# Optimization experiments

Hardware: AMD Instinct MI355X
Metric: run time of the kernel (lower is better)

Reference implementation:

```python
import jax, jax.numpy as jnp
import numpy as np

B, S, D, H, DFF = 4, 1024, 1024, 16, 4096
MAX_LEN = 1024
DK = D // H
EPS = 1e-5


def _ln(x, g, b):
    m = jnp.mean(x, axis=-1, keepdims=True)
    v = jnp.mean(jnp.square(x - m), axis=-1, keepdims=True)
    return (x - m) / jnp.sqrt(v + EPS) * g + b


def setup_inputs() -> dict:
    key = jax.random.key(0)
    ks = jax.random.split(key, 16)
    s = 0.02
    inp = {
        "x": jax.random.normal(ks[0], (B, S, D), jnp.float32),
        "wq": jax.random.normal(ks[1], (D, D), jnp.float32) * s,
        "bq": jnp.zeros((D,), jnp.float32),
        "wk": jax.random.normal(ks[2], (D, D), jnp.float32) * s,
        "bk": jnp.zeros((D,), jnp.float32),
        "wv": jax.random.normal(ks[3], (D, D), jnp.float32) * s,
        "bv": jnp.zeros((D,), jnp.float32),
        "wo": jax.random.normal(ks[4], (D, D), jnp.float32) * s,
        "bo": jnp.zeros((D,), jnp.float32),
        "rel_table": jax.random.normal(ks[5], (2 * MAX_LEN - 1, H), jnp.float32) * s,
        "ln1_g": jnp.ones((D,), jnp.float32),
        "ln1_b": jnp.zeros((D,), jnp.float32),
        "w1": jax.random.normal(ks[6], (D, DFF), jnp.float32) * s,
        "b1": jnp.zeros((DFF,), jnp.float32),
        "w2": jax.random.normal(ks[7], (DFF, D), jnp.float32) * s,
        "b2": jnp.zeros((D,), jnp.float32),
        "ln2_g": jnp.ones((D,), jnp.float32),
        "ln2_b": jnp.zeros((D,), jnp.float32),
        "mask": jnp.ones((B, 1, 1, S), jnp.int32),
    }
    return inp


def reference(x, wq, bq, wk, bk, wv, bv, wo, bo, rel_table,
              ln1_g, ln1_b, w1, b1, w2, b2, ln2_g, ln2_b, mask):
    # --- multi-head attention with relative position bias (post-LN encoder layer, eval mode) ---
    q = (x @ wq + bq).reshape(B, S, H, DK).transpose(0, 2, 1, 3)  # [B,H,S,dk]
    k = (x @ wk + bk).reshape(B, S, H, DK).transpose(0, 2, 1, 3)
    v = (x @ wv + bv).reshape(B, S, H, DK).transpose(0, 2, 1, 3)

    scores = jnp.einsum('bhqd,bhkd->bhqk', q, k) / jnp.sqrt(jnp.float32(DK))

    # relative position bias: table[(q - k + max_len - 1).clip] -> [1,H,S,S]
    coords = jnp.arange(S)[:, None] - jnp.arange(S)[None, :] + (MAX_LEN - 1)
    coords = jnp.clip(coords, 0, 2 * MAX_LEN - 2)
    bias = rel_table[coords]              # [S,S,H]
    scores = scores + bias.transpose(2, 0, 1)[None]

    scores = jnp.where(mask == 0, jnp.float32(-1e9), scores)
    attn = jax.nn.softmax(scores, axis=-1)
    ctx = jnp.einsum('bhqk,bhkd->bhqd', attn, v)
    ctx = ctx.transpose(0, 2, 1, 3).reshape(B, S, D)
    attn_out = ctx @ wo + bo

    x1 = _ln(x + attn_out, ln1_g, ln1_b)

    ff = jax.nn.relu(x1 @ w1 + b1) @ w2 + b2
    return _ln(x1 + ff, ln2_g, ln2_b)
```

## Files before the change

kernel.cpp:

```cpp
#include <hip/hip_runtime.h>
#include <hip/hip_bf16.h>

typedef __hip_bfloat16 bf16;
typedef __attribute__((ext_vector_type(8))) short short8;
typedef __attribute__((ext_vector_type(4))) float f32x4;

#define LOG2E 1.4426950408889634f

typedef const __attribute__((address_space(1))) void* gptr_t;
typedef __attribute__((address_space(3))) void* sptr_t;

__device__ __forceinline__ void async16(void* lds, const void* g) {
  __builtin_amdgcn_global_load_lds((gptr_t)g, (sptr_t)lds, 16, 0, 0);
}

__device__ __forceinline__ float bf2f(unsigned short u) {
  union { unsigned int i; float f; } c; c.i = ((unsigned int)u) << 16; return c.f;
}


__global__ __launch_bounds__(256) void prep_all(
    const float* __restrict__ x, const float* __restrict__ bq,
    const float* __restrict__ bk, const float* __restrict__ bv,
    const float* __restrict__ wq, const float* __restrict__ wk,
    const float* __restrict__ wv, const float* __restrict__ wo,
    const float* __restrict__ w1, const float* __restrict__ w2,
    bf16* __restrict__ xb, float* __restrict__ bqkv,
    bf16* __restrict__ dqkv, bf16* __restrict__ dwo,
    bf16* __restrict__ dw1, bf16* __restrict__ dw2) {
  const int bid = blockIdx.x;
  if (bid < 4096) {
    int i = (bid * 256 + threadIdx.x) * 4;
    float4 v = *(const float4*)(x + i);
    bf16 h4[4] = {__float2bfloat16(v.x), __float2bfloat16(v.y),
                  __float2bfloat16(v.z), __float2bfloat16(v.w)};
    *(uint2*)((unsigned short*)xb + i) = *(uint2*)h4;
    return;
  }
  if (bid == 16384) {
#pragma unroll
    for (int j = 0; j < 12; ++j) {
      int i = j * 256 + threadIdx.x;
      bqkv[i] = (i < 1024) ? bq[i] : (i < 2048 ? bk[i - 1024] : bv[i - 2048]);
    }
    return;
  }
  __shared__ float tl[32][33];
  const int tid = bid - 4096;
  const float* s;
  bf16* d;
  int NN, KK, n0, k0;
  if (tid < 4096) {
    int m = tid >> 10, tile = tid & 1023;
    s = m == 0 ? wq : m == 1 ? wk : m == 2 ? wv : wo;
    d = m < 3 ? dqkv + (size_t)m * 1024 * 1024 : dwo;
    NN = 1024; KK = 1024;
    n0 = (tile & 31) * 32; k0 = (tile >> 5) * 32;
  } else if (tid < 8192) {
    int tile = tid - 4096;
    s = w1; d = dw1; NN = 4096; KK = 1024;
    n0 = (tile & 127) * 32; k0 = (tile >> 7) * 32;
  } else {
    int tile = tid - 8192;
    s = w2; d = dw2; NN = 1024; KK = 4096;
    n0 = (tile & 31) * 32; k0 = (tile >> 5) * 32;
  }
  const int tx = threadIdx.x & 31, ty = threadIdx.x >> 5;
#pragma unroll
  for (int j = 0; j < 4; ++j)
    tl[ty + j * 8][tx] = s[(size_t)(k0 + ty + j * 8) * NN + n0 + tx];
  __syncthreads();
#pragma unroll
  for (int j = 0; j < 4; ++j)
    d[(size_t)(n0 + ty + j * 8) * KK + k0 + tx] =
        __float2bfloat16(tl[tx][ty + j * 8]);
}

__global__ __launch_bounds__(256) void build_vt(
    const bf16* __restrict__ qkv, bf16* __restrict__ vt) {
  __shared__ bf16 tl[32][33];
  const int bhz = blockIdx.z, s0 = blockIdx.x * 32, dk0 = blockIdx.y * 32;
  const int b = bhz >> 4, h = bhz & 15;
  const int tx = threadIdx.x, ty = threadIdx.y;
#pragma unroll
  for (int j = 0; j < 4; ++j) {
    int s = s0 + ty + j * 8;
    tl[ty + j * 8][tx] =
        qkv[(size_t)(b * 1024 + s) * 3072 + 2048 + h * 64 + dk0 + tx];
  }
  __syncthreads();
#pragma unroll
  for (int j = 0; j < 4; ++j) {
    int dk = dk0 + ty + j * 8;
    vt[(size_t)(bhz * 64 + dk) * 1024 + s0 + tx] = tl[tx][ty + j * 8];
  }
}


template <int RELU>
__global__ __launch_bounds__(256) void gemm_bt(
    const bf16* __restrict__ A, const bf16* __restrict__ Bt,
    const float* __restrict__ bias, bf16* __restrict__ C, int M, int N, int K) {
  __shared__ bf16 As[2][128 * 64];
  __shared__ bf16 Bs[2][128 * 64];
  const int t = threadIdx.x;
  const int w = t >> 6, l = t & 63;
  const int m0 = blockIdx.y * 128, n0 = blockIdx.x * 128;
  const int wr = (w >> 1) * 64, wc = (w & 1) * 64;
  const int srow = l >> 3, scol = l & 7;
  const int lm = l & 15, lq = l >> 4;

  f32x4 acc[4][4];
#pragma unroll
  for (int i = 0; i < 4; ++i)
#pragma unroll
    for (int j = 0; j < 4; ++j) acc[i][j] = (f32x4){0.f, 0.f, 0.f, 0.f};

  auto stage = [&](int k0, int d) {
#pragma unroll
    for (int p = 0; p < 4; ++p) {
      int row = p * 32 + w * 8 + srow;
      int gc = scol ^ (row & 7);
      async16(&As[d][(p * 32 + w * 8) * 64], A + (size_t)(m0 + row) * K + k0 + gc * 8);
      async16(&Bs[d][(p * 32 + w * 8) * 64], Bt + (size_t)(n0 + row) * K + k0 + gc * 8);
    }
  };

  stage(0, 0);
  const int niter = K >> 6;
  for (int it = 0; it < niter; ++it) {
    const int d = it & 1;
    __syncthreads();
    short8 af[2][4], bfr[2][4];
#pragma unroll
    for (int kk = 0; kk < 2; ++kk)
#pragma unroll
      for (int mi = 0; mi < 4; ++mi) {
        int rowa = wr + mi * 16 + lm;
        af[kk][mi] = *(const short8*)&As[d][rowa * 64 + (((kk * 4 + lq) ^ (rowa & 7)) << 3)];
        int rowb = wc + mi * 16 + lm;
        bfr[kk][mi] = *(const short8*)&Bs[d][rowb * 64 + (((kk * 4 + lq) ^ (rowb & 7)) << 3)];
      }
    if (it + 1 < niter) stage((it + 1) << 6, d ^ 1);
#pragma unroll
    for (int kk = 0; kk < 2; ++kk)
#pragma unroll
      for (int mi = 0; mi < 4; ++mi)
#pragma unroll
        for (int ni = 0; ni < 4; ++ni)
          acc[mi][ni] = __builtin_amdgcn_mfma_f32_16x16x32_bf16(
              af[kk][mi], bfr[kk][ni], acc[mi][ni], 0, 0, 0);
  }
#pragma unroll
  for (int mi = 0; mi < 4; ++mi)
#pragma unroll
    for (int r = 0; r < 4; ++r) {
      int row = m0 + wr + mi * 16 + lq * 4 + r;
#pragma unroll
      for (int ni = 0; ni < 4; ++ni) {
        int col = n0 + wc + ni * 16 + lm;
        float v = acc[mi][ni][r] + bias[col];
        if (RELU) v = fmaxf(v, 0.f);
        C[(size_t)row * N + col] = __float2bfloat16(v);
      }
    }
}

template <typename OT>
__global__ __launch_bounds__(256) void gemm_bt_splitk(
    const bf16* __restrict__ A, const bf16* __restrict__ Bt,
    OT* __restrict__ P, int M, int N, int lda, int KS) {
  __shared__ bf16 As[2][128 * 64];
  __shared__ bf16 Bs[2][128 * 64];
  const int t = threadIdx.x;
  const int w = t >> 6, l = t & 63;
  const int m0 = blockIdx.y * 128, n0 = blockIdx.x * 128;
  const int kstart = blockIdx.z * KS;
  const int wr = (w >> 1) * 64, wc = (w & 1) * 64;
  const int srow = l >> 3, scol = l & 7;
  const int lm = l & 15, lq = l >> 4;

  f32x4 acc[4][4];
#pragma unroll
  for (int i = 0; i < 4; ++i)
#pragma unroll
    for (int j = 0; j < 4; ++j) acc[i][j] = (f32x4){0.f, 0.f, 0.f, 0.f};

  auto stage = [&](int k0, int d) {
#pragma unroll
    for (int p = 0; p < 4; ++p) {
      int row = p * 32 + w * 8 + srow;
      int gc = scol ^ (row & 7);
      async16(&As[d][(p * 32 + w * 8) * 64], A + (size_t)(m0 + row) * lda + k0 + gc * 8);
      async16(&Bs[d][(p * 32 + w * 8) * 64], Bt + (size_t)(n0 + row) * lda + k0 + gc * 8);
    }
  };

  stage(kstart, 0);
  const int niter = KS >> 6;
  for (int it = 0; it < niter; ++it) {
    const int d = it & 1;
    __syncthreads();
    short8 af[2][4], bfr[2][4];
#pragma unroll
    for (int kk = 0; kk < 2; ++kk)
#pragma unroll
      for (int mi = 0; mi < 4; ++mi) {
        int rowa = wr + mi * 16 + lm;
        af[kk][mi] = *(const short8*)&As[d][rowa * 64 + (((kk * 4 + lq) ^ (rowa & 7)) << 3)];
        int rowb = wc + mi * 16 + lm;
        bfr[kk][mi] = *(const short8*)&Bs[d][rowb * 64 + (((kk * 4 + lq) ^ (rowb & 7)) << 3)];
      }
    if (it + 1 < niter) stage(kstart + ((it + 1) << 6), d ^ 1);
#pragma unroll
    for (int kk = 0; kk < 2; ++kk)
#pragma unroll
      for (int mi = 0; mi < 4; ++mi)
#pragma unroll
        for (int ni = 0; ni < 4; ++ni)
          acc[mi][ni] = __builtin_amdgcn_mfma_f32_16x16x32_bf16(
              af[kk][mi], bfr[kk][ni], acc[mi][ni], 0, 0, 0);
  }
  OT* Pz = P + (size_t)blockIdx.z * M * N;
#pragma unroll
  for (int mi = 0; mi < 4; ++mi)
#pragma unroll
    for (int r = 0; r < 4; ++r) {
      int row = m0 + wr + mi * 16 + lq * 4 + r;
#pragma unroll
      for (int ni = 0; ni < 4; ++ni) {
        int col = n0 + wc + ni * 16 + lm;
        float v = acc[mi][ni][r];
        if constexpr (sizeof(OT) == 4)
          Pz[(size_t)row * N + col] = v;
        else
          Pz[(size_t)row * N + col] = __float2bfloat16(v);
      }
    }
}


__global__ __launch_bounds__(512, 4) void flash_attn(
    const bf16* __restrict__ qkv, const bf16* __restrict__ vt,
    const float* __restrict__ rel, const int* __restrict__ mask,
    bf16* __restrict__ ctx) {
  __shared__ bf16 Kl[2][64 * 64];
  __shared__ bf16 Vl[2][64 * 64];
  __shared__ bf16 Pl[128 * 64];
  __shared__ float bias_s[2][192];
  __shared__ float mask_s[2][64];

  const int t = threadIdx.x;
  const int w = t >> 6, l = t & 63;
  const int lm = l & 15, lq = l >> 4;
  const int qt = blockIdx.x, bh = blockIdx.y;
  const int b = bh >> 4, h = bh & 15;
  const int q0 = qt * 128;
  const int srow = l >> 3;
  const int gc = (l & 7) ^ srow;
  const int qq = w * 16 + lm;

  auto stage = [&](int d, int k0n) {
    async16(&Kl[d][w * 8 * 64],
            qkv + (size_t)(b * 1024 + k0n + w * 8 + srow) * 3072 + 1024 + h * 64 + gc * 8);
    async16(&Vl[d][w * 8 * 64],
            vt + ((size_t)bh * 64 + w * 8 + srow) * 1024 + k0n + gc * 8);
    if (t < 191) bias_s[d][t] = rel[(q0 - k0n + 960 + t) * 16 + h] * LOG2E;
    if (t < 64) mask_s[d][t] = (mask[b * 1024 + k0n + t] == 0) ? -1.44e9f : 0.f;
  };

#pragma unroll
  for (int p = 0; p < 2; ++p)
    async16(&Pl[(p * 64 + w * 8) * 64],
            qkv + (size_t)(b * 1024 + q0 + p * 64 + w * 8 + srow) * 3072 + h * 64 + gc * 8);
  stage(0, 0);
  __syncthreads();

  short8 qf[2];
#pragma unroll
  for (int kk = 0; kk < 2; ++kk)
    qf[kk] = *(const short8*)&Pl[qq * 64 + (((kk * 4 + lq) ^ (lm & 7)) << 3)];
  __syncthreads();

  float l_acc = 0.f;
  f32x4 acc_o[4];
#pragma unroll
  for (int j = 0; j < 4; ++j) acc_o[j] = (f32x4){0.f, 0.f, 0.f, 0.f};

  const float C0 = 0.125f * LOG2E;

  for (int kt = 0; kt < 16; ++kt) {
    const int d = kt & 1;
    if (kt < 15) stage(d ^ 1, (kt + 1) * 64);

    f32x4 sa[4];
#pragma unroll
    for (int i = 0; i < 4; ++i) sa[i] = (f32x4){0.f, 0.f, 0.f, 0.f};
#pragma unroll
    for (int kk = 0; kk < 2; ++kk) {
      short8 ak[4];
#pragma unroll
      for (int mi = 0; mi < 4; ++mi) {
        int row = mi * 16 + lm;
        ak[mi] = *(const short8*)&Kl[d][row * 64 + (((kk * 4 + lq) ^ (lm & 7)) << 3)];
      }
#pragma unroll
      for (int mi = 0; mi < 4; ++mi)
        sa[mi] = __builtin_amdgcn_mfma_f32_16x16x32_bf16(ak[mi], qf[kk], sa[mi], 0, 0, 0);
    }

    float m4[4][4];
#pragma unroll
    for (int mi = 0; mi < 4; ++mi)
      *(float4*)m4[mi] = *(const float4*)&mask_s[d][mi * 16 + lq * 4];
#pragma unroll
    for (int mi = 0; mi < 4; ++mi)
#pragma unroll
      for (int r = 0; r < 4; ++r) {
        int kl = mi * 16 + lq * 4 + r;
        float p = __builtin_amdgcn_exp2f(
            fmaf(sa[mi][r], C0, bias_s[d][qq - kl + 63] + m4[mi][r]));
        sa[mi][r] = p;
        l_acc += p;
      }

#pragma unroll
    for (int mi = 0; mi < 4; ++mi) {
      bf16 h4[4];
#pragma unroll
      for (int r = 0; r < 4; ++r) h4[r] = __float2bfloat16(sa[mi][r]);
      int chunk = mi * 2 + (lq >> 1);
      *(uint2*)&Pl[qq * 64 + ((chunk ^ (lm & 7)) << 3) + ((lq & 1) << 2)] =
          *(uint2*)h4;
    }

#pragma unroll
    for (int kk2 = 0; kk2 < 2; ++kk2) {
      short8 pf = *(const short8*)&Pl[qq * 64 + (((kk2 * 4 + lq) ^ (lm & 7)) << 3)];
      short8 vf[4];
#pragma unroll
      for (int ni = 0; ni < 4; ++ni) {
        int rowv = ni * 16 + lm;
        vf[ni] = *(const short8*)&Vl[d][rowv * 64 + (((kk2 * 4 + lq) ^ (lm & 7)) << 3)];
      }
#pragma unroll
      for (int ni = 0; ni < 4; ++ni)
        acc_o[ni] = __builtin_amdgcn_mfma_f32_16x16x32_bf16(pf, vf[ni], acc_o[ni], 0, 0, 0);
    }
    __syncthreads();
  }

  l_acc += __shfl_xor(l_acc, 16);
  l_acc += __shfl_xor(l_acc, 32);
  float linv = 1.f / l_acc;
#pragma unroll
  for (int r = 0; r < 4; ++r) {
    float il = __shfl(linv, lq * 4 + r);
    int qx = w * 16 + lq * 4 + r;
    size_t rowbase = (size_t)(b * 1024 + q0 + qx) * 1024 + h * 64;
#pragma unroll
    for (int ni = 0; ni < 4; ++ni)
      ctx[rowbase + ni * 16 + lm] = __float2bfloat16(acc_o[ni][r] * il);
  }
}


template <typename PT, int NS>
__global__ __launch_bounds__(256) void ln_resid(
    const float* __restrict__ xin, const PT* __restrict__ part,
    const float* __restrict__ bias,
    const float* __restrict__ gw, const float* __restrict__ bw,
    float* __restrict__ outf, bf16* __restrict__ outb) {
  const int row = blockIdx.x, t = threadIdx.x;
  const size_t base = (size_t)row * 1024 + t * 4;
  float4 xv = *(const float4*)(xin + base);
  float4 bi = *(const float4*)(bias + t * 4);
  float v0 = xv.x + bi.x, v1 = xv.y + bi.y, v2 = xv.z + bi.z, v3 = xv.w + bi.w;
#pragma unroll
  for (int s = 0; s < NS; ++s) {
    const PT* p = part + (size_t)s * 4194304 + base;
    if constexpr (sizeof(PT) == 4) {
      float4 pv = *(const float4*)p;
      v0 += pv.x; v1 += pv.y; v2 += pv.z; v3 += pv.w;
    } else {
      ushort4 pv = *(const ushort4*)p;
      v0 += bf2f(pv.x); v1 += bf2f(pv.y); v2 += bf2f(pv.z); v3 += bf2f(pv.w);
    }
  }
  float s1 = v0 + v1 + v2 + v3;
  float s2 = v0 * v0 + v1 * v1 + v2 * v2 + v3 * v3;
#pragma unroll
  for (int o = 1; o < 64; o <<= 1) {
    s1 += __shfl_xor(s1, o);
    s2 += __shfl_xor(s2, o);
  }
  __shared__ float red[8];
  const int w = t >> 6, l = t & 63;
  if (l == 0) { red[w] = s1; red[4 + w] = s2; }
  __syncthreads();
  float S1 = red[0] + red[1] + red[2] + red[3];
  float S2 = red[4] + red[5] + red[6] + red[7];
  float mean = S1 * (1.f / 1024.f);
  float var = S2 * (1.f / 1024.f) - mean * mean;
  float rstd = rsqrtf(var + 1e-5f);
  float4 gv = *(const float4*)(gw + t * 4);
  float4 bv = *(const float4*)(bw + t * 4);
  float o0 = (v0 - mean) * rstd * gv.x + bv.x;
  float o1 = (v1 - mean) * rstd * gv.y + bv.y;
  float o2 = (v2 - mean) * rstd * gv.z + bv.z;
  float o3 = (v3 - mean) * rstd * gv.w + bv.w;
  if (outf) {
    float4 ov = {o0, o1, o2, o3};
    *(float4*)(outf + base) = ov;
  }
  if (outb) {
    bf16 h4[4] = {__float2bfloat16(o0), __float2bfloat16(o1),
                  __float2bfloat16(o2), __float2bfloat16(o3)};
    *(uint2*)((unsigned short*)outb + base) = *(uint2*)h4;
  }
}


extern "C" void kernel_launch(void* const* d_in, const int* in_sizes, int n_in,
                              void* d_out, int out_size, void* d_ws, size_t ws_size,
                              hipStream_t stream) {
  (void)in_sizes; (void)n_in; (void)out_size; (void)ws_size;
  const float* x   = (const float*)d_in[0];
  const float* wq  = (const float*)d_in[1];
  const float* bq  = (const float*)d_in[2];
  const float* wk  = (const float*)d_in[3];
  const float* bk  = (const float*)d_in[4];
  const float* wv  = (const float*)d_in[5];
  const float* bv  = (const float*)d_in[6];
  const float* wo  = (const float*)d_in[7];
  const float* bo  = (const float*)d_in[8];
  const float* rel = (const float*)d_in[9];
  const float* g1  = (const float*)d_in[10];
  const float* be1 = (const float*)d_in[11];
  const float* w1  = (const float*)d_in[12];
  const float* b1  = (const float*)d_in[13];
  const float* w2  = (const float*)d_in[14];
  const float* b2  = (const float*)d_in[15];
  const float* g2  = (const float*)d_in[16];
  const float* be2 = (const float*)d_in[17];
  const int* mask  = (const int*)d_in[18];
  float* out = (float*)d_out;

  char* ws = (char*)d_ws;
  bf16*  xb      = (bf16*)(ws + 0);
  bf16*  wqkv_t  = (bf16*)(ws + 8388608);
  bf16*  wo_t    = (bf16*)(ws + 14680064);
  bf16*  w1_t    = (bf16*)(ws + 16777216);
  bf16*  ctx_b   = (bf16*)(ws + 25165824);
  bf16*  x1b     = (bf16*)(ws + 33554432);
  bf16*  qkv_b   = (bf16*)(ws + 41943040);
  bf16*  vtb     = (bf16*)(ws + 67108864);
  bf16*  part_wo = (bf16*)(ws + 41943040);
  bf16*  h1      = (bf16*)(ws + 41943040);
  bf16*  part_ff = (bf16*)(ws + 0);
  bf16*  w2_t    = (bf16*)(ws + 75497472);
  float* x1f     = (float*)(ws + 83886080);
  float* bqkv    = (float*)(ws + 100663296);

  dim3 tb(32, 8);
  prep_all<<<16385, 256, 0, stream>>>(x, bq, bk, bv, wq, wk, wv, wo, w1, w2,
                                      xb, bqkv, wqkv_t, wo_t, w1_t, w2_t);

  gemm_bt<0><<<dim3(24, 32), 256, 0, stream>>>(xb, wqkv_t, bqkv, qkv_b, 4096, 3072, 1024);
  build_vt<<<dim3(32, 2, 64), tb, 0, stream>>>(qkv_b, vtb);
  flash_attn<<<dim3(8, 64), 512, 0, stream>>>(qkv_b, vtb, rel, mask, ctx_b);
  gemm_bt_splitk<bf16><<<dim3(8, 32, 2), 256, 0, stream>>>(
      ctx_b, wo_t, part_wo, 4096, 1024, 1024, 512);
  ln_resid<bf16, 2><<<4096, 256, 0, stream>>>(x, part_wo, bo, g1, be1, x1f, x1b);
  gemm_bt<1><<<dim3(32, 32), 256, 0, stream>>>(x1b, w1_t, b1, h1, 4096, 4096, 1024);
  gemm_bt_splitk<bf16><<<dim3(8, 32, 2), 256, 0, stream>>>(
      h1, w2_t, part_ff, 4096, 1024, 4096, 2048);
  ln_resid<bf16, 2><<<4096, 256, 0, stream>>>(x1f, part_ff, b2, g2, be2, out, nullptr);
}
```

Baseline: 316.6 us.

## Fuse V transpose into QKV GEMM epilogue, halve K tile, raise split-K

Removes the separate build_vt kernel: the QKV GEMM epilogue now also writes the transposed V layout directly, using 8-byte stores of four consecutive sequence positions. Both GEMM kernels drop the K tile from 64 to 32, which halves shared memory, and declare launch bounds targeting four blocks per CU. The grid is swapped so M tiles run along x. The output-projection and FFN2 GEMMs now split K four ways instead of two, and the LayerNorm kernels sum four bf16 partials. This trades one kernel launch and a V round trip, plus better occupancy and parallelism, for more barriers per unit of K and extra partial-sum traffic.

```diff
diff --git a/kernel.cpp b/kernel.cpp
--- a/kernel.cpp
+++ b/kernel.cpp
@@ -76,38 +76,19 @@
         __float2bfloat16(tl[tx][ty + j * 8]);
 }
 
-__global__ __launch_bounds__(256) void build_vt(
-    const bf16* __restrict__ qkv, bf16* __restrict__ vt) {
-  __shared__ bf16 tl[32][33];
-  const int bhz = blockIdx.z, s0 = blockIdx.x * 32, dk0 = blockIdx.y * 32;
-  const int b = bhz >> 4, h = bhz & 15;
-  const int tx = threadIdx.x, ty = threadIdx.y;
-#pragma unroll
-  for (int j = 0; j < 4; ++j) {
-    int s = s0 + ty + j * 8;
-    tl[ty + j * 8][tx] =
-        qkv[(size_t)(b * 1024 + s) * 3072 + 2048 + h * 64 + dk0 + tx];
-  }
-  __syncthreads();
-#pragma unroll
-  for (int j = 0; j < 4; ++j) {
-    int dk = dk0 + ty + j * 8;
-    vt[(size_t)(bhz * 64 + dk) * 1024 + s0 + tx] = tl[tx][ty + j * 8];
-  }
-}
-
-
-template <int RELU>
-__global__ __launch_bounds__(256) void gemm_bt(
+
+template <int RELU, int VT>
+__global__ __launch_bounds__(256, 4) void gemm_bt(
     const bf16* __restrict__ A, const bf16* __restrict__ Bt,
-    const float* __restrict__ bias, bf16* __restrict__ C, int M, int N, int K) {
-  __shared__ bf16 As[2][128 * 64];
-  __shared__ bf16 Bs[2][128 * 64];
+    const float* __restrict__ bias, bf16* __restrict__ C,
+    bf16* __restrict__ vt, int M, int N, int K) {
+  __shared__ bf16 As[2][128 * 32];
+  __shared__ bf16 Bs[2][128 * 32];
   const int t = threadIdx.x;
   const int w = t >> 6, l = t & 63;
-  const int m0 = blockIdx.y * 128, n0 = blockIdx.x * 128;
+  const int m0 = blockIdx.x * 128, n0 = blockIdx.y * 128;
   const int wr = (w >> 1) * 64, wc = (w & 1) * 64;
-  const int srow = l >> 3, scol = l & 7;
+  const int srow = l >> 2, schunk = l & 3;
   const int lm = l & 15, lq = l >> 4;
 
   f32x4 acc[4][4];
@@ -118,66 +99,74 @@
 
   auto stage = [&](int k0, int d) {
 #pragma unroll
-    for (int p = 0; p < 4; ++p) {
-      int row = p * 32 + w * 8 + srow;
-      int gc = scol ^ (row & 7);
-      async16(&As[d][(p * 32 + w * 8) * 64], A + (size_t)(m0 + row) * K + k0 + gc * 8);
-      async16(&Bs[d][(p * 32 + w * 8) * 64], Bt + (size_t)(n0 + row) * K + k0 + gc * 8);
+    for (int p = 0; p < 2; ++p) {
+      int rbase = p * 64 + w * 16;
+      int row = rbase + srow;
+      int gc = schunk ^ (row & 3);
+      async16(&As[d][rbase * 32], A + (size_t)(m0 + row) * K + k0 + gc * 8);
+      async16(&Bs[d][rbase * 32], Bt + (size_t)(n0 + row) * K + k0 + gc * 8);
     }
   };
 
   stage(0, 0);
-  const int niter = K >> 6;
+  const int niter = K >> 5;
   for (int it = 0; it < niter; ++it) {
     const int d = it & 1;
     __syncthreads();
-    short8 af[2][4], bfr[2][4];
-#pragma unroll
-    for (int kk = 0; kk < 2; ++kk)
-#pragma unroll
-      for (int mi = 0; mi < 4; ++mi) {
-        int rowa = wr + mi * 16 + lm;
-        af[kk][mi] = *(const short8*)&As[d][rowa * 64 + (((kk * 4 + lq) ^ (rowa & 7)) << 3)];
-        int rowb = wc + mi * 16 + lm;
-        bfr[kk][mi] = *(const short8*)&Bs[d][rowb * 64 + (((kk * 4 + lq) ^ (rowb & 7)) << 3)];
-      }
-    if (it + 1 < niter) stage((it + 1) << 6, d ^ 1);
-#pragma unroll
-    for (int kk = 0; kk < 2; ++kk)
-#pragma unroll
-      for (int mi = 0; mi < 4; ++mi)
-#pragma unroll
-        for (int ni = 0; ni < 4; ++ni)
-          acc[mi][ni] = __builtin_amdgcn_mfma_f32_16x16x32_bf16(
-              af[kk][mi], bfr[kk][ni], acc[mi][ni], 0, 0, 0);
-  }
+    short8 af[4], bfr[4];
+#pragma unroll
+    for (int mi = 0; mi < 4; ++mi) {
+      int rowa = wr + mi * 16 + lm;
+      af[mi] = *(const short8*)&As[d][rowa * 32 + ((lq ^ (rowa & 3)) << 3)];
+      int rowb = wc + mi * 16 + lm;
+      bfr[mi] = *(const short8*)&Bs[d][rowb * 32 + ((lq ^ (rowb & 3)) << 3)];
+    }
+    if (it + 1 < niter) stage((it + 1) << 5, d ^ 1);
+#pragma unroll
+    for (int mi = 0; mi < 4; ++mi)
+#pragma unroll
+      for (int ni = 0; ni < 4; ++ni)
+        acc[mi][ni] = __builtin_amdgcn_mfma_f32_16x16x32_bf16(
+            af[mi], bfr[ni], acc[mi][ni], 0, 0, 0);
+  }
+
 #pragma unroll
   for (int mi = 0; mi < 4; ++mi)
 #pragma unroll
-    for (int r = 0; r < 4; ++r) {
-      int row = m0 + wr + mi * 16 + lq * 4 + r;
-#pragma unroll
-      for (int ni = 0; ni < 4; ++ni) {
-        int col = n0 + wc + ni * 16 + lm;
-        float v = acc[mi][ni][r] + bias[col];
-        if (RELU) v = fmaxf(v, 0.f);
-        C[(size_t)row * N + col] = __float2bfloat16(v);
-      }
-    }
-}
-
-template <typename OT>
-__global__ __launch_bounds__(256) void gemm_bt_splitk(
+    for (int ni = 0; ni < 4; ++ni) {
+      int col = n0 + wc + ni * 16 + lm;
+      int row0 = m0 + wr + mi * 16 + lq * 4;
+      float bv = bias[col];
+      float v[4];
+#pragma unroll
+      for (int r = 0; r < 4; ++r) {
+        v[r] = acc[mi][ni][r] + bv;
+        if (RELU) v[r] = fmaxf(v[r], 0.f);
+        C[(size_t)(row0 + r) * N + col] = __float2bfloat16(v[r]);
+      }
+      if (VT && col >= 2048) {
+        int vcol = col - 2048;
+        int bh = (row0 >> 10) * 16 + (vcol >> 6);
+        int dk = vcol & 63;
+        int s = row0 & 1023;
+        bf16 h4[4] = {__float2bfloat16(v[0]), __float2bfloat16(v[1]),
+                      __float2bfloat16(v[2]), __float2bfloat16(v[3])};
+        *(uint2*)&vt[((size_t)bh * 64 + dk) * 1024 + s] = *(uint2*)h4;
+      }
+    }
+}
+
+__global__ __launch_bounds__(256, 4) void gemm_bt_splitk(
     const bf16* __restrict__ A, const bf16* __restrict__ Bt,
-    OT* __restrict__ P, int M, int N, int lda, int KS) {
-  __shared__ bf16 As[2][128 * 64];
-  __shared__ bf16 Bs[2][128 * 64];
+    bf16* __restrict__ P, int M, int N, int lda, int KS) {
+  __shared__ bf16 As[2][128 * 32];
+  __shared__ bf16 Bs[2][128 * 32];
   const int t = threadIdx.x;
   const int w = t >> 6, l = t & 63;
-  const int m0 = blockIdx.y * 128, n0 = blockIdx.x * 128;
+  const int m0 = blockIdx.x * 128, n0 = blockIdx.y * 128;
   const int kstart = blockIdx.z * KS;
   const int wr = (w >> 1) * 64, wc = (w & 1) * 64;
-  const int srow = l >> 3, scol = l & 7;
+  const int srow = l >> 2, schunk = l & 3;
   const int lm = l & 15, lq = l >> 4;
 
   f32x4 acc[4][4];
@@ -188,40 +177,37 @@
 
   auto stage = [&](int k0, int d) {
 #pragma unroll
-    for (int p = 0; p < 4; ++p) {
-      int row = p * 32 + w * 8 + srow;
-      int gc = scol ^ (row & 7);
-      async16(&As[d][(p * 32 + w * 8) * 64], A + (size_t)(m0 + row) * lda + k0 + gc * 8);
-      async16(&Bs[d][(p * 32 + w * 8) * 64], Bt + (size_t)(n0 + row) * lda + k0 + gc * 8);
+    for (int p = 0; p < 2; ++p) {
+      int rbase = p * 64 + w * 16;
+      int row = rbase + srow;
+      int gc = schunk ^ (row & 3);
+      async16(&As[d][rbase * 32], A + (size_t)(m0 + row) * lda + k0 + gc * 8);
+      async16(&Bs[d][rbase * 32], Bt + (size_t)(n0 + row) * lda + k0 + gc * 8);
     }
   };
 
   stage(kstart, 0);
-  const int niter = KS >> 6;
+  const int niter = KS >> 5;
   for (int it = 0; it < niter; ++it) {
     const int d = it & 1;
     __syncthreads();
-    short8 af[2][4], bfr[2][4];
-#pragma unroll
-    for (int kk = 0; kk < 2; ++kk)
-#pragma unroll
-      for (int mi = 0; mi < 4; ++mi) {
-        int rowa = wr + mi * 16 + lm;
-        af[kk][mi] = *(const short8*)&As[d][rowa * 64 + (((kk * 4 + lq) ^ (rowa & 7)) << 3)];
-        int rowb = wc + mi * 16 + lm;
-        bfr[kk][mi] = *(const short8*)&Bs[d][rowb * 64 + (((kk * 4 + lq) ^ (rowb & 7)) << 3)];
-      }
-    if (it + 1 < niter) stage(kstart + ((it + 1) << 6), d ^ 1);
-#pragma unroll
-    for (int kk = 0; kk < 2; ++kk)
-#pragma unroll
-      for (int mi = 0; mi < 4; ++mi)
-#pragma unroll
-        for (int ni = 0; ni < 4; ++ni)
-          acc[mi][ni] = __builtin_amdgcn_mfma_f32_16x16x32_bf16(
-              af[kk][mi], bfr[kk][ni], acc[mi][ni], 0, 0, 0);
-  }
-  OT* Pz = P + (size_t)blockIdx.z * M * N;
+    short8 af[4], bfr[4];
+#pragma unroll
+    for (int mi = 0; mi < 4; ++mi) {
+      int rowa = wr + mi * 16 + lm;
+      af[mi] = *(const short8*)&As[d][rowa * 32 + ((lq ^ (rowa & 3)) << 3)];
+      int rowb = wc + mi * 16 + lm;
+      bfr[mi] = *(const short8*)&Bs[d][rowb * 32 + ((lq ^ (rowb & 3)) << 3)];
+    }
+    if (it + 1 < niter) stage(kstart + ((it + 1) << 5), d ^ 1);
+#pragma unroll
+    for (int mi = 0; mi < 4; ++mi)
+#pragma unroll
+      for (int ni = 0; ni < 4; ++ni)
+        acc[mi][ni] = __builtin_amdgcn_mfma_f32_16x16x32_bf16(
+            af[mi], bfr[ni], acc[mi][ni], 0, 0, 0);
+  }
+  bf16* Pz = P + (size_t)blockIdx.z * M * N;
 #pragma unroll
   for (int mi = 0; mi < 4; ++mi)
 #pragma unroll
@@ -230,11 +216,7 @@
 #pragma unroll
       for (int ni = 0; ni < 4; ++ni) {
         int col = n0 + wc + ni * 16 + lm;
-        float v = acc[mi][ni][r];
-        if constexpr (sizeof(OT) == 4)
-          Pz[(size_t)row * N + col] = v;
-        else
-          Pz[(size_t)row * N + col] = __float2bfloat16(v);
+        Pz[(size_t)row * N + col] = __float2bfloat16(acc[mi][ni][r]);
       }
     }
 }
@@ -365,9 +347,9 @@
 }
 
 
-template <typename PT, int NS>
+template <int NS>
 __global__ __launch_bounds__(256) void ln_resid(
-    const float* __restrict__ xin, const PT* __restrict__ part,
+    const float* __restrict__ xin, const bf16* __restrict__ part,
     const float* __restrict__ bias,
     const float* __restrict__ gw, const float* __restrict__ bw,
     float* __restrict__ outf, bf16* __restrict__ outb) {
@@ -378,14 +360,9 @@
   float v0 = xv.x + bi.x, v1 = xv.y + bi.y, v2 = xv.z + bi.z, v3 = xv.w + bi.w;
 #pragma unroll
   for (int s = 0; s < NS; ++s) {
-    const PT* p = part + (size_t)s * 4194304 + base;
-    if constexpr (sizeof(PT) == 4) {
-      float4 pv = *(const float4*)p;
-      v0 += pv.x; v1 += pv.y; v2 += pv.z; v3 += pv.w;
-    } else {
-      ushort4 pv = *(const ushort4*)p;
-      v0 += bf2f(pv.x); v1 += bf2f(pv.y); v2 += bf2f(pv.z); v3 += bf2f(pv.w);
-    }
+    const bf16* p = part + (size_t)s * 4194304 + base;
+    ushort4 pv = *(const ushort4*)p;
+    v0 += bf2f(pv.x); v1 += bf2f(pv.y); v2 += bf2f(pv.z); v3 += bf2f(pv.w);
   }
   float s1 = v0 + v1 + v2 + v3;
   float s2 = v0 * v0 + v1 * v1 + v2 * v2 + v3 * v3;
@@ -462,18 +439,18 @@
   float* x1f     = (float*)(ws + 83886080);
   float* bqkv    = (float*)(ws + 100663296);
 
-  dim3 tb(32, 8);
   prep_all<<<16385, 256, 0, stream>>>(x, bq, bk, bv, wq, wk, wv, wo, w1, w2,
                                       xb, bqkv, wqkv_t, wo_t, w1_t, w2_t);
 
-  gemm_bt<0><<<dim3(24, 32), 256, 0, stream>>>(xb, wqkv_t, bqkv, qkv_b, 4096, 3072, 1024);
-  build_vt<<<dim3(32, 2, 64), tb, 0, stream>>>(qkv_b, vtb);
+  gemm_bt<0, 1><<<dim3(32, 24), 256, 0, stream>>>(
+      xb, wqkv_t, bqkv, qkv_b, vtb, 4096, 3072, 1024);
   flash_attn<<<dim3(8, 64), 512, 0, stream>>>(qkv_b, vtb, rel, mask, ctx_b);
-  gemm_bt_splitk<bf16><<<dim3(8, 32, 2), 256, 0, stream>>>(
-      ctx_b, wo_t, part_wo, 4096, 1024, 1024, 512);
-  ln_resid<bf16, 2><<<4096, 256, 0, stream>>>(x, part_wo, bo, g1, be1, x1f, x1b);
-  gemm_bt<1><<<dim3(32, 32), 256, 0, stream>>>(x1b, w1_t, b1, h1, 4096, 4096, 1024);
-  gemm_bt_splitk<bf16><<<dim3(8, 32, 2), 256, 0, stream>>>(
-      h1, w2_t, part_ff, 4096, 1024, 4096, 2048);
-  ln_resid<bf16, 2><<<4096, 256, 0, stream>>>(x1f, part_ff, b2, g2, be2, out, nullptr);
-}
+  gemm_bt_splitk<<<dim3(32, 8, 4), 256, 0, stream>>>(
+      ctx_b, wo_t, part_wo, 4096, 1024, 1024, 256);
+  ln_resid<4><<<4096, 256, 0, stream>>>(x, part_wo, bo, g1, be1, x1f, x1b);
+  gemm_bt<1, 0><<<dim3(32, 32), 256, 0, stream>>>(
+      x1b, w1_t, b1, h1, nullptr, 4096, 4096, 1024);
+  gemm_bt_splitk<<<dim3(32, 8, 4), 256, 0, stream>>>(
+      h1, w2_t, part_ff, 4096, 1024, 4096, 1024);
+  ln_resid<4><<<4096, 256, 0, stream>>>(x1f, part_ff, b2, g2, be2, out, nullptr);
+}
```

Measured after the change: 336.0 us. 6.1% more time.
